# Performance work log

Measured on AMD Instinct MI355X. Metric: run time of the kernel, lower is better.

The kernel has to match this reference:

```python
import jax, jax.numpy as jnp
import numpy as np


def setup_inputs() -> dict:
    key = jax.random.key(0)
    ks = jax.random.split(key, 8)
    b, m, e, d = 8, 4096, 2048, 128
    features = jax.random.normal(ks[0], (b, m, d), dtype=jnp.float32)
    # sparse-ish binary incidence matrix (nodes x hyperedges)
    inc_mat = (jax.random.uniform(ks[1], (b, m, e)) < 0.02).astype(jnp.float32)
    s = 1.0 / np.sqrt(d)
    return {
        "features": features,
        "inc_mat": inc_mat,
        "vc_Wa": jax.random.uniform(ks[2], (d, d), minval=-s, maxval=s),
        "vc_Wp": jax.random.uniform(ks[3], (d, d), minval=-s, maxval=s),
        "vc_alpha": jnp.float32(0.5),
        "ec_Wa": jax.random.uniform(ks[4], (d, d), minval=-s, maxval=s),
        "ec_Wp": jax.random.uniform(ks[5], (d, d), minval=-s, maxval=s),
        "ec_alpha": jnp.float32(0.5),
        "n_layers": 3,
    }


def _vertex_conv(feat, inc, Wa, Wp, alpha, prev=None):
    # feat: [b,m,d], inc: [b,m,e]
    att = feat @ Wa.T                                   # [b,m,d]
    e_att = jnp.einsum('bme,bmd->bed', inc, att)        # inc^T @ att
    attw = jax.nn.softmax(e_att, axis=1)                # softmax over edges
    agg = jnp.einsum('bme,bmd->bed', inc, feat)         # collapsed bmed outer-product + contract
    ef = (agg * attw) @ Wp.T                            # [b,e,d]
    if prev is not None:
        ef = alpha * prev + (1.0 - alpha) * ef
    return ef


def _edge_conv(inc, edge_feats, Wa, Wp, alpha, prev=None):
    # NOTE: original EdgeConv computes softmax attention_weights but never uses them (dead code).
    w = jnp.einsum('bed,bme->bmd', edge_feats, inc)     # inc @ edge_feats
    nf = w @ Wp.T                                       # [b,m,d]
    if prev is not None:
        nf = alpha * prev + (1.0 - alpha) * nf
    return nf


def reference(features, inc_mat, vc_Wa, vc_Wp, vc_alpha, ec_Wa, ec_Wp, ec_alpha, n_layers):
    edge_feats = _vertex_conv(features, inc_mat, vc_Wa, vc_Wp, vc_alpha)
    node_feats = _edge_conv(inc_mat, edge_feats, ec_Wa, ec_Wp, ec_alpha)
    for _ in range(1, n_layers):
        edge_feats = _vertex_conv(features, inc_mat, vc_Wa, vc_Wp, vc_alpha, prev=edge_feats)
        node_feats = _edge_conv(inc_mat, edge_feats, ec_Wa, ec_Wp, ec_alpha, prev=node_feats)
    return node_feats, edge_feats
```

## Files before the change

kernel.cpp:

```cpp
#include <hip/hip_runtime.h>

#define BB 8
#define MM 4096
#define EE 2048
#define DD 128

typedef _Float16 f16x8 __attribute__((ext_vector_type(8)));
typedef float    f32x4 __attribute__((ext_vector_type(4)));

__global__ __launch_bounds__(256) void pack_both(const float* __restrict__ inc,
                                                 unsigned long long* __restrict__ bits,
                                                 unsigned long long* __restrict__ bitsT)
{
    const int b  = blockIdx.z;
    const int w  = threadIdx.x >> 6;
    const int lane = threadIdx.x & 63;
    const int m0 = (blockIdx.y * 4 + w) * 64;
    const int e0 = blockIdx.x * 64;
    const float* ip = inc + ((size_t)b * MM + m0) * EE + e0;

    unsigned long long wbits = 0;
    #pragma unroll
    for (int mi = 0; mi < 64; mi++){
        float v = ip[(size_t)mi * EE + lane];
        unsigned long long bal = __ballot(v != 0.0f);
        wbits = (lane == mi) ? bal : wbits;
    }
    bits[((size_t)b * MM + m0 + lane) * (EE / 64) + (e0 >> 6)] = wbits;

    unsigned long long wT = 0;
    #pragma unroll
    for (int ei = 0; ei < 64; ei++){
        unsigned long long bal = __ballot((wbits >> ei) & 1ull);
        wT = (lane == ei) ? bal : wT;
    }
    bitsT[((size_t)b * EE + e0 + lane) * (MM / 64) + (m0 >> 6)] = wT;
}

__global__ __launch_bounds__(256) void transpose_to16(const float* __restrict__ src,
                                                      _Float16* __restrict__ dst,
                                                      int R, int C)
{
    __shared__ alignas(16) float tile[64 * 67];
    const int tilesC = C >> 6;
    const int r0 = (blockIdx.x / tilesC) << 6;
    const int c0 = (blockIdx.x % tilesC) << 6;
    const float* s = src + (size_t)blockIdx.y * R * C;
    _Float16*   d = dst + (size_t)blockIdx.y * R * C;
    const int t = threadIdx.x;
    #pragma unroll
    for (int i = 0; i < 4; i++){
        int idx = t + 256 * i;
        int r = idx >> 4, c4 = idx & 15;
        float4 v = *(const float4*)(s + (size_t)(r0 + r) * C + c0 + c4 * 4);
        tile[(c4 * 4 + 0) * 67 + r] = v.x;
        tile[(c4 * 4 + 1) * 67 + r] = v.y;
        tile[(c4 * 4 + 2) * 67 + r] = v.z;
        tile[(c4 * 4 + 3) * 67 + r] = v.w;
    }
    __syncthreads();
    #pragma unroll
    for (int i = 0; i < 2; i++){
        int idx = t + 256 * i;
        int row = idx >> 3, rb = idx & 7;
        f16x8 h;
        #pragma unroll
        for (int j = 0; j < 8; j++) h[j] = (_Float16)tile[row * 67 + rb * 8 + j];
        *(f16x8*)(d + (size_t)(c0 + row) * R + r0 + rb * 8) = h;
    }
}

__global__ __launch_bounds__(256) void bitgemm1(const uint2* __restrict__ bitrows,
                                                const _Float16* __restrict__ dense,
                                                float* __restrict__ out)
{
    __shared__ alignas(16) char smem[33792];
    const int b = blockIdx.y;
    const int row0 = blockIdx.x * 64;
    const int WB = MM >> 6;
    const uint2* bp = bitrows + ((size_t)b * EE + row0) * WB;
    const _Float16* dp = dense + (size_t)b * 128 * MM;
    float* op = out + (size_t)blockIdx.z * 2097152 + ((size_t)b * EE + row0) * 128;
    const int kbase = blockIdx.z * 2048;

    const int t = threadIdx.x, lane = t & 63, w = t >> 6;
    const int fr = lane & 15, q = lane >> 4, q8 = q * 8;

    f32x4 acc[8] = {};
    uint4 rd[4];
    uint2 rb;

    auto loadg = [&](int kg){
        #pragma unroll
        for (int i = 0; i < 4; i++){
            int idx = t + 256 * i;
            int dd = idx >> 3, kb = idx & 7;
            rd[i] = *(const uint4*)(dp + (size_t)dd * MM + kg + kb * 8);
        }
        if (t < 64) rb = bp[(size_t)t * WB + (kg >> 6)];
    };
    auto stage = [&](int buf){
        _Float16* lD = (_Float16*)(smem + buf * 16384);
        uint2* lB = (uint2*)(smem + 32768 + buf * 512);
        #pragma unroll
        for (int i = 0; i < 4; i++){
            int idx = t + 256 * i;
            int dd = idx >> 3, kb = idx & 7;
            *(uint4*)&lD[dd * 64 + ((kb ^ (dd & 7)) * 8)] = rd[i];
        }
        if (t < 64) lB[t] = rb;
    };
    auto compute = [&](int buf){
        const _Float16* lD = (const _Float16*)(smem + buf * 16384);
        const uint2* lB = (const uint2*)(smem + 32768 + buf * 512);
        uint2 bw = lB[w * 16 + fr];
        #pragma unroll
        for (int h = 0; h < 2; h++){
            unsigned word = h ? bw.y : bw.x;
            unsigned byte = (word >> q8) & 0xFFu;
            f16x8 af;
            #pragma unroll
            for (int j = 0; j < 8; j++)
                af[j] = ((byte >> j) & 1u) ? (_Float16)1.0f : (_Float16)0.0f;
            #pragma unroll
            for (int c = 0; c < 8; c++){
                int drow = c * 16 + fr;
                f16x8 bf = *(const f16x8*)&lD[drow * 64 + (((h * 4 + q) ^ (drow & 7)) * 8)];
                acc[c] = __builtin_amdgcn_mfma_f32_16x16x32_f16(af, bf, acc[c], 0, 0, 0);
            }
        }
    };

    loadg(kbase); stage(0); __syncthreads();
    for (int c = 0; c < 32; c++){
        if (c + 1 < 32) loadg(kbase + (c + 1) * 64);
        compute(c & 1);
        if (c + 1 < 32) stage((c + 1) & 1);
        __syncthreads();
    }
    float* sT = (float*)smem;
    #pragma unroll
    for (int c = 0; c < 8; c++)
        #pragma unroll
        for (int reg = 0; reg < 4; reg++)
            sT[(w * 16 + q * 4 + reg) * 132 + c * 16 + fr] = acc[c][reg];
    __syncthreads();
    #pragma unroll
    for (int i = 0; i < 8; i++){
        int idx = t + 256 * i;
        int lrow = idx >> 5, c4 = idx & 31;
        float4 v = *(const float4*)&sT[lrow * 132 + c4 * 4];
        *(float4*)(op + (size_t)lrow * 128 + c4 * 4) = v;
    }
}

__global__ __launch_bounds__(256) void bitgemm2_fused(const uint2* __restrict__ bitrows,
                                                      const _Float16* __restrict__ PT,
                                                      const _Float16* __restrict__ Wc16,
                                                      float* __restrict__ node)
{
    __shared__ alignas(16) char smem[66560];
    const int b = blockIdx.y;
    const int m0 = blockIdx.x * 64;
    const int WB = EE >> 6;
    const uint2* bp = bitrows + ((size_t)b * MM + m0) * WB;
    const _Float16* dp = PT + (size_t)b * 128 * EE;
    float* op = node + ((size_t)b * MM + m0) * 128;

    const int t = threadIdx.x, lane = t & 63, w = t >> 6;
    const int fr = lane & 15, q = lane >> 4, q8 = q * 8;

    _Float16* lWc = (_Float16*)(smem + 33792);
    #pragma unroll
    for (int i = 0; i < 8; i++){
        int idx = t + 256 * i;
        int n = idx >> 4, kb = idx & 15;
        *(uint4*)&lWc[n * 128 + ((kb ^ (n & 7)) * 8)] =
            *(const uint4*)(Wc16 + (size_t)n * 128 + kb * 8);
    }

    f32x4 acc[8] = {};
    uint4 rd[4];
    uint2 rb;

    auto loadg = [&](int kg){
        #pragma unroll
        for (int i = 0; i < 4; i++){
            int idx = t + 256 * i;
            int dd = idx >> 3, kb = idx & 7;
            rd[i] = *(const uint4*)(dp + (size_t)dd * EE + kg + kb * 8);
        }
        if (t < 64) rb = bp[(size_t)t * WB + (kg >> 6)];
    };
    auto stage = [&](int buf){
        _Float16* lD = (_Float16*)(smem + buf * 16384);
        uint2* lB = (uint2*)(smem + 32768 + buf * 512);
        #pragma unroll
        for (int i = 0; i < 4; i++){
            int idx = t + 256 * i;
            int dd = idx >> 3, kb = idx & 7;
            *(uint4*)&lD[dd * 64 + ((kb ^ (dd & 7)) * 8)] = rd[i];
        }
        if (t < 64) lB[t] = rb;
    };
    auto compute = [&](int buf){
        const _Float16* lD = (const _Float16*)(smem + buf * 16384);
        const uint2* lB = (const uint2*)(smem + 32768 + buf * 512);
        uint2 bw = lB[w * 16 + fr];
        #pragma unroll
        for (int h = 0; h < 2; h++){
            unsigned word = h ? bw.y : bw.x;
            unsigned byte = (word >> q8) & 0xFFu;
            f16x8 af;
            #pragma unroll
            for (int j = 0; j < 8; j++)
                af[j] = ((byte >> j) & 1u) ? (_Float16)1.0f : (_Float16)0.0f;
            #pragma unroll
            for (int c = 0; c < 8; c++){
                int drow = c * 16 + fr;
                f16x8 bf = *(const f16x8*)&lD[drow * 64 + (((h * 4 + q) ^ (drow & 7)) * 8)];
                acc[c] = __builtin_amdgcn_mfma_f32_16x16x32_f16(af, bf, acc[c], 0, 0, 0);
            }
        }
    };

    loadg(0); stage(0); __syncthreads();
    for (int c = 0; c < 32; c++){
        if (c + 1 < 32) loadg((c + 1) * 64);
        compute(c & 1);
        if (c + 1 < 32) stage((c + 1) & 1);
        __syncthreads();
    }

    _Float16* sQ = (_Float16*)smem;
    #pragma unroll
    for (int c = 0; c < 8; c++){
        #pragma unroll
        for (int reg = 0; reg < 4; reg++){
            int row = w * 16 + q * 4 + reg;
            int col = c * 16 + fr;
            sQ[row * 128 + (((col >> 3) ^ (row & 7)) * 8) + (col & 7)] = (_Float16)acc[c][reg];
        }
    }
    f32x4 acc2[8] = {};
    #pragma unroll
    for (int kk = 0; kk < 4; kk++){
        int arow = w * 16 + fr;
        f16x8 a2 = *(const f16x8*)&sQ[arow * 128 + (((kk * 4 + q) ^ (arow & 7)) * 8)];
        #pragma unroll
        for (int c = 0; c < 8; c++){
            int n = c * 16 + fr;
            f16x8 b2 = *(const f16x8*)&lWc[n * 128 + (((kk * 4 + q) ^ (n & 7)) * 8)];
            acc2[c] = __builtin_amdgcn_mfma_f32_16x16x32_f16(a2, b2, acc2[c], 0, 0, 0);
        }
    }
    __syncthreads();
    float* sD = (float*)smem;
    #pragma unroll
    for (int c = 0; c < 8; c++)
        #pragma unroll
        for (int reg = 0; reg < 4; reg++)
            sD[(w * 16 + q * 4 + reg) * 132 + c * 16 + fr] = acc2[c][reg];
    __syncthreads();
    #pragma unroll
    for (int i = 0; i < 8; i++){
        int idx = t + 256 * i;
        int lrow = idx >> 5, c4 = idx & 31;
        float4 v = *(const float4*)&sD[lrow * 132 + c4 * 4];
        *(float4*)(op + (size_t)lrow * 128 + c4 * 4) = v;
    }
}

__global__ __launch_bounds__(256) void rowmm_sum2(const float* __restrict__ p,
                                                  const float* __restrict__ W,
                                                  float* aggOut,
                                                  float* __restrict__ C)
{
    __shared__ alignas(16) float lA[32][132];
    __shared__ alignas(16) float lW[64][140];
    const int t = threadIdx.x;
    const int row0 = blockIdx.x * 32;
    const float4* P4 = (const float4*)p;
    const float4* W4 = (const float4*)W;
    float4* A4 = (float4*)aggOut;
    const size_t SS = 2097152 / 4;

    #pragma unroll
    for (int i = 0; i < 4; i++){
        int idx = t + 256 * i;
        int r = idx >> 5, k4 = idx & 31;
        size_t gi = (size_t)(row0 + r) * 32 + k4;
        float4 a = P4[gi], b = P4[gi + SS];
        float4 s = make_float4(a.x + b.x, a.y + b.y, a.z + b.z, a.w + b.w);
        *(float4*)&lA[r][k4 * 4] = s;
        A4[gi] = s;
    }
    const int qq = t >> 5, cc = t & 31;

    #pragma unroll
    for (int ph = 0; ph < 2; ph++){
        __syncthreads();
        #pragma unroll
        for (int i = 0; i < 8; i++){
            int idx = t + 256 * i;
            int c = idx >> 5, k4 = idx & 31;
            *(float4*)&lW[c][k4 * 4] = W4[(size_t)(ph * 64 + c) * 32 + k4];
        }
        __syncthreads();
        float s[4][2] = {};
        for (int k4 = 0; k4 < 32; k4++){
            float4 w0 = *(const float4*)&lW[cc][k4 * 4];
            float4 w1 = *(const float4*)&lW[cc + 32][k4 * 4];
            #pragma unroll
            for (int j = 0; j < 4; j++){
                float4 a = *(const float4*)&lA[qq + 8 * j][k4 * 4];
                s[j][0] += a.x * w0.x + a.y * w0.y + a.z * w0.z + a.w * w0.w;
                s[j][1] += a.x * w1.x + a.y * w1.y + a.z * w1.z + a.w * w1.w;
            }
        }
        #pragma unroll
        for (int j = 0; j < 4; j++){
            size_t ro = (size_t)(row0 + qq + 8 * j) * DD + ph * 64;
            C[ro + cc]      = s[j][0];
            C[ro + cc + 32] = s[j][1];
        }
    }
}

__global__ __launch_bounds__(256) void rowmm(const float* A,
                                             const float* __restrict__ W,
                                             float* C)
{
    __shared__ alignas(16) float lA[32][132];
    __shared__ alignas(16) float lW[64][140];
    const int t = threadIdx.x;
    const int row0 = blockIdx.x * 32;
    const float4* A4 = (const float4*)A;
    const float4* W4 = (const float4*)W;

    #pragma unroll
    for (int i = 0; i < 4; i++){
        int idx = t + 256 * i;
        int r = idx >> 5, k4 = idx & 31;
        *(float4*)&lA[r][k4 * 4] = A4[(size_t)(row0 + r) * 32 + k4];
    }
    const int qq = t >> 5, cc = t & 31;

    #pragma unroll
    for (int ph = 0; ph < 2; ph++){
        __syncthreads();
        #pragma unroll
        for (int i = 0; i < 8; i++){
            int idx = t + 256 * i;
            int c = idx >> 5, k4 = idx & 31;
            *(float4*)&lW[c][k4 * 4] = W4[(size_t)(ph * 64 + c) * 32 + k4];
        }
        __syncthreads();
        float s[4][2] = {};
        for (int k4 = 0; k4 < 32; k4++){
            float4 w0 = *(const float4*)&lW[cc][k4 * 4];
            float4 w1 = *(const float4*)&lW[cc + 32][k4 * 4];
            #pragma unroll
            for (int j = 0; j < 4; j++){
                float4 a = *(const float4*)&lA[qq + 8 * j][k4 * 4];
                s[j][0] += a.x * w0.x + a.y * w0.y + a.z * w0.z + a.w * w0.w;
                s[j][1] += a.x * w1.x + a.y * w1.y + a.z * w1.z + a.w * w1.w;
            }
        }
        #pragma unroll
        for (int j = 0; j < 4; j++){
            size_t ro = (size_t)(row0 + qq + 8 * j) * DD + ph * 64;
            C[ro + cc]      = s[j][0];
            C[ro + cc + 32] = s[j][1];
        }
    }
}

__global__ __launch_bounds__(256) void wc_mm16(const float* __restrict__ eWp,
                                               const float* __restrict__ vWp,
                                               _Float16* __restrict__ Wc16)
{
    int i = blockIdx.x * 2 + (threadIdx.x >> 7);
    int j = threadIdx.x & 127;
    float acc = 0.f;
    for (int k = 0; k < 128; k++)
        acc += eWp[i * 128 + k] * vWp[k * 128 + j];
    Wc16[i * 128 + j] = (_Float16)acc;
}

__global__ __launch_bounds__(256) void sm_part(const float* __restrict__ eatt,
                                               float* __restrict__ part)
{
    const int b = blockIdx.x, slab = blockIdx.y;
    const int t = threadIdx.x;
    const int dl = t & 127, eh = t >> 7;
    const size_t base = (size_t)b * EE * DD + dl;
    const int e0 = slab * 256;
    float m = -1e30f;
    for (int s = 0; s < 128; s++)
        m = fmaxf(m, eatt[base + (size_t)(e0 + eh + 2 * s) * DD]);
    float l = 0.f;
    for (int s = 0; s < 128; s++)
        l += __expf(eatt[base + (size_t)(e0 + eh + 2 * s) * DD] - m);
    __shared__ float red[2][128][2];
    red[eh][dl][0] = m; red[eh][dl][1] = l;
    __syncthreads();
    if (t < 128){
        float m0 = red[0][t][0], l0 = red[0][t][1];
        float m1 = red[1][t][0], l1 = red[1][t][1];
        float M = fmaxf(m0, m1);
        float L = l0 * __expf(m0 - M) + l1 * __expf(m1 - M);
        float* pp = part + ((size_t)(b * 8 + slab) * DD + t) * 2;
        pp[0] = M; pp[1] = L;
    }
}

__global__ __launch_bounds__(256) void sm_apply(float* __restrict__ eatt,
                                                const float* __restrict__ agg,
                                                const float* __restrict__ part)
{
    const int b = blockIdx.x, sl = blockIdx.y;
    const int t = threadIdx.x;
    __shared__ float mv[128], iv[128];
    if (t < 128){
        float mbuf[8], lbuf[8];
        float M = -1e30f;
        #pragma unroll
        for (int s = 0; s < 8; s++){
            const float* pp = part + ((size_t)(b * 8 + s) * DD + t) * 2;
            mbuf[s] = pp[0]; lbuf[s] = pp[1];
            M = fmaxf(M, mbuf[s]);
        }
        float L = 0.f;
        #pragma unroll
        for (int s = 0; s < 8; s++) L += lbuf[s] * __expf(mbuf[s] - M);
        mv[t] = M; iv[t] = 1.f / L;
    }
    __syncthreads();
    const int dl = t & 127, eh = t >> 7;
    const size_t base = (size_t)b * EE * DD + dl;
    const int e0 = sl * 128;
    for (int s = 0; s < 64; s++){
        size_t ix = base + (size_t)(e0 + eh + 2 * s) * DD;
        eatt[ix] = agg[ix] * __expf(eatt[ix] - mv[dl]) * iv[dl];
    }
}

extern "C" void kernel_launch(void* const* d_in, const int* in_sizes, int n_in,
                              void* d_out, int out_size, void* d_ws, size_t ws_size,
                              hipStream_t stream)
{
    const float* feat = (const float*)d_in[0];
    const float* inc  = (const float*)d_in[1];
    const float* vWa  = (const float*)d_in[2];
    const float* vWp  = (const float*)d_in[3];
    const float* eWp  = (const float*)d_in[6];

    float* node_out = (float*)d_out;
    float* edge_out = node_out + (size_t)BB * MM * DD;

    char* w = (char*)d_ws;
    unsigned long long* bits  = (unsigned long long*)w;
    unsigned long long* bitsT = (unsigned long long*)(w + ((size_t)8 << 20));
    _Float16* PT = (_Float16*)(w + ((size_t)8 << 20));
    float* pk  = (float*)(w + ((size_t)16 << 20));
    float* agg = pk;
    _Float16* Wc16 = (_Float16*)(w + ((size_t)32 << 20));

    _Float16* featT = (_Float16*)node_out;
    float* eattP = node_out + 2097152;
    float* part  = edge_out;

    dim3 blk(256);

    pack_both<<<dim3(EE / 64, MM / 256, BB), blk, 0, stream>>>(inc, bits, bitsT);
    transpose_to16<<<dim3((MM / 64) * (DD / 64), BB), blk, 0, stream>>>(feat, featT, MM, DD);
    wc_mm16<<<dim3(64), blk, 0, stream>>>(eWp, vWp, Wc16);
    bitgemm1<<<dim3(EE / 64, BB, 2), blk, 0, stream>>>((const uint2*)bitsT, featT, pk);
    rowmm_sum2<<<dim3(BB * EE / 32), blk, 0, stream>>>(pk, vWa, agg, eattP);
    sm_part <<<dim3(BB, 8),  blk, 0, stream>>>(eattP, part);
    sm_apply<<<dim3(BB, 16), blk, 0, stream>>>(eattP, agg, part);
    rowmm<<<dim3(BB * EE / 32), blk, 0, stream>>>(eattP, vWp, edge_out);
    transpose_to16<<<dim3((EE / 64) * (DD / 64), BB), blk, 0, stream>>>(eattP, PT, EE, DD);
    bitgemm2_fused<<<dim3(MM / 64, BB), blk, 0, stream>>>((const uint2*)bits, PT, Wc16, node_out);
}
```

Baseline: 618.7 us.

## Fuse incidence bit-packing into first bit-GEMM with 4-way K split

Removes the separate pack_both kernel and has the first GEMM read the float incidence matrix directly. It ballots the values into bit masks, transposes them in registers for its own MFMA A operand, and writes a column-major bit layout for the second GEMM. Each block now covers 256 edges with a 4-way K split, and the partial-sum reducer is widened from 2 to 4 slices. This avoids a second pass over the bit data, but it raises register pressure (64 staged floats plus 32 accumulators, launch bound of 1 block) and gives fewer blocks per batch.

```diff
diff --git a/kernel.cpp b/kernel.cpp
--- a/kernel.cpp
+++ b/kernel.cpp
@@ -7,35 +7,6 @@
 
 typedef _Float16 f16x8 __attribute__((ext_vector_type(8)));
 typedef float    f32x4 __attribute__((ext_vector_type(4)));
-
-__global__ __launch_bounds__(256) void pack_both(const float* __restrict__ inc,
-                                                 unsigned long long* __restrict__ bits,
-                                                 unsigned long long* __restrict__ bitsT)
-{
-    const int b  = blockIdx.z;
-    const int w  = threadIdx.x >> 6;
-    const int lane = threadIdx.x & 63;
-    const int m0 = (blockIdx.y * 4 + w) * 64;
-    const int e0 = blockIdx.x * 64;
-    const float* ip = inc + ((size_t)b * MM + m0) * EE + e0;
-
-    unsigned long long wbits = 0;
-    #pragma unroll
-    for (int mi = 0; mi < 64; mi++){
-        float v = ip[(size_t)mi * EE + lane];
-        unsigned long long bal = __ballot(v != 0.0f);
-        wbits = (lane == mi) ? bal : wbits;
-    }
-    bits[((size_t)b * MM + m0 + lane) * (EE / 64) + (e0 >> 6)] = wbits;
-
-    unsigned long long wT = 0;
-    #pragma unroll
-    for (int ei = 0; ei < 64; ei++){
-        unsigned long long bal = __ballot((wbits >> ei) & 1ull);
-        wT = (lane == ei) ? bal : wT;
-    }
-    bitsT[((size_t)b * EE + e0 + lane) * (MM / 64) + (m0 >> 6)] = wT;
-}
 
 __global__ __launch_bounds__(256) void transpose_to16(const float* __restrict__ src,
                                                       _Float16* __restrict__ dst,
@@ -70,38 +41,166 @@
     }
 }
 
-__global__ __launch_bounds__(256) void bitgemm1(const uint2* __restrict__ bitrows,
-                                                const _Float16* __restrict__ dense,
-                                                float* __restrict__ out)
-{
-    __shared__ alignas(16) char smem[33792];
+__global__ __launch_bounds__(256, 1) void fused_gemm1(const float* __restrict__ inc,
+                                                      const _Float16* __restrict__ featT,
+                                                      unsigned long long* __restrict__ bitsX,
+                                                      float* __restrict__ p)
+{
+    __shared__ alignas(16) char smem[36864];
+
+    const int x = blockIdx.x;
     const int b = blockIdx.y;
-    const int row0 = blockIdx.x * 64;
-    const int WB = MM >> 6;
-    const uint2* bp = bitrows + ((size_t)b * EE + row0) * WB;
-    const _Float16* dp = dense + (size_t)b * 128 * MM;
-    float* op = out + (size_t)blockIdx.z * 2097152 + ((size_t)b * EE + row0) * 128;
-    const int kbase = blockIdx.z * 2048;
-
+    const int z = blockIdx.z;
     const int t = threadIdx.x, lane = t & 63, w = t >> 6;
     const int fr = lane & 15, q = lane >> 4, q8 = q * 8;
 
+    const int e0 = x * 256;
+    const int ew0 = e0 + w * 64;
+    const _Float16* dp = featT + (size_t)b * 128 * MM;
+    const float* ip = inc + (size_t)b * MM * EE + ew0 + lane;
+    unsigned long long* bxp = bitsX + ((size_t)b * 32 + (x * 4 + w)) * MM;
+
+    f32x4 acc[4][8] = {};
+    uint4 rd[4];
+    float val[64];
+
+    auto loadg = [&](int k0){
+        #pragma unroll
+        for (int i = 0; i < 4; i++){
+            int idx = t + 256 * i;
+            int dd = idx >> 3, kb = idx & 7;
+            rd[i] = *(const uint4*)(dp + (size_t)dd * MM + k0 + kb * 8);
+        }
+        const float* rp = ip + (size_t)k0 * EE;
+        #pragma unroll
+        for (int j = 0; j < 64; j++) val[j] = rp[(size_t)j * EE];
+    };
+    auto stage = [&](int buf, int k0){
+        _Float16* lD = (_Float16*)(smem + buf * 16384);
+        unsigned long long* lBits = (unsigned long long*)(smem + 32768 + buf * 2048);
+        #pragma unroll
+        for (int i = 0; i < 4; i++){
+            int idx = t + 256 * i;
+            int dd = idx >> 3, kb = idx & 7;
+            *(uint4*)&lD[dd * 64 + ((kb ^ (dd & 7)) * 8)] = rd[i];
+        }
+        unsigned long long wbits = 0;
+        #pragma unroll
+        for (int j = 0; j < 64; j++){
+            unsigned long long bal = __ballot(val[j] != 0.0f);
+            wbits = (lane == j) ? bal : wbits;
+        }
+        bxp[k0 + lane] = wbits;
+        unsigned long long wT = 0;
+        #pragma unroll
+        for (int ei = 0; ei < 64; ei++){
+            unsigned long long bal = __ballot((wbits >> ei) & 1ull);
+            wT = (lane == ei) ? bal : wT;
+        }
+        lBits[w * 64 + lane] = wT;
+    };
+    auto compute = [&](int buf){
+        const _Float16* lD = (const _Float16*)(smem + buf * 16384);
+        const uint2* lBits = (const uint2*)(smem + 32768 + buf * 2048);
+        uint2 bw[4];
+        f16x8 af[4][2];
+        #pragma unroll
+        for (int s = 0; s < 4; s++) bw[s] = lBits[w * 64 + s * 16 + fr];
+        #pragma unroll
+        for (int s = 0; s < 4; s++)
+            #pragma unroll
+            for (int h = 0; h < 2; h++){
+                unsigned word = h ? bw[s].y : bw[s].x;
+                unsigned byte = (word >> q8) & 0xFFu;
+                #pragma unroll
+                for (int j = 0; j < 8; j++)
+                    af[s][h][j] = ((byte >> j) & 1u) ? (_Float16)1.0f : (_Float16)0.0f;
+            }
+        #pragma unroll
+        for (int h = 0; h < 2; h++)
+            #pragma unroll
+            for (int c = 0; c < 8; c++){
+                int drow = c * 16 + fr;
+                f16x8 bf = *(const f16x8*)&lD[drow * 64 + (((h * 4 + q) ^ (drow & 7)) * 8)];
+                #pragma unroll
+                for (int s = 0; s < 4; s++)
+                    acc[s][c] = __builtin_amdgcn_mfma_f32_16x16x32_f16(af[s][h], bf, acc[s][c], 0, 0, 0);
+            }
+    };
+
+    const int kbase = z * 1024;
+    loadg(kbase); stage(0, kbase); __syncthreads();
+    for (int c = 0; c < 16; c++){
+        if (c + 1 < 16) loadg(kbase + (c + 1) * 64);
+        compute(c & 1);
+        if (c + 1 < 16) stage((c + 1) & 1, kbase + (c + 1) * 64);
+        __syncthreads();
+    }
+
+    float* sT = (float*)smem;
+    float* op = p + (size_t)z * 2097152 + ((size_t)b * EE + e0) * 128;
+    for (int ph = 0; ph < 4; ph++){
+        __syncthreads();
+        if (w == ph){
+            #pragma unroll
+            for (int s = 0; s < 4; s++)
+                #pragma unroll
+                for (int c = 0; c < 8; c++)
+                    #pragma unroll
+                    for (int reg = 0; reg < 4; reg++)
+                        sT[(s * 16 + q * 4 + reg) * 132 + c * 16 + fr] = acc[s][c][reg];
+        }
+        __syncthreads();
+        #pragma unroll
+        for (int i = 0; i < 8; i++){
+            int idx = t + 256 * i;
+            int lrow = idx >> 5, c4 = idx & 31;
+            float4 v = *(const float4*)&sT[lrow * 132 + c4 * 4];
+            *(float4*)(op + (size_t)(ph * 64 + lrow) * 128 + c4 * 4) = v;
+        }
+    }
+}
+
+__global__ __launch_bounds__(256) void bitgemm2_fused(const unsigned long long* __restrict__ bitsX,
+                                                      const _Float16* __restrict__ PT,
+                                                      const _Float16* __restrict__ Wc16,
+                                                      float* __restrict__ node)
+{
+    __shared__ alignas(16) char smem[66560];
+    const int b = blockIdx.y;
+    const int m0 = blockIdx.x * 64;
+    const unsigned long long* bxp = bitsX + (size_t)b * 32 * MM;
+    const _Float16* dp = PT + (size_t)b * 128 * EE;
+    float* op = node + ((size_t)b * MM + m0) * 128;
+
+    const int t = threadIdx.x, lane = t & 63, w = t >> 6;
+    const int fr = lane & 15, q = lane >> 4, q8 = q * 8;
+
+    _Float16* lWc = (_Float16*)(smem + 33792);
+    #pragma unroll
+    for (int i = 0; i < 8; i++){
+        int idx = t + 256 * i;
+        int n = idx >> 4, kb = idx & 15;
+        *(uint4*)&lWc[n * 128 + ((kb ^ (n & 7)) * 8)] =
+            *(const uint4*)(Wc16 + (size_t)n * 128 + kb * 8);
+    }
+
     f32x4 acc[8] = {};
     uint4 rd[4];
-    uint2 rb;
+    unsigned long long rb;
 
     auto loadg = [&](int kg){
         #pragma unroll
         for (int i = 0; i < 4; i++){
             int idx = t + 256 * i;
             int dd = idx >> 3, kb = idx & 7;
-            rd[i] = *(const uint4*)(dp + (size_t)dd * MM + kg + kb * 8);
-        }
-        if (t < 64) rb = bp[(size_t)t * WB + (kg >> 6)];
+            rd[i] = *(const uint4*)(dp + (size_t)dd * EE + kg + kb * 8);
+        }
+        if (t < 64) rb = bxp[(size_t)(kg >> 6) * MM + m0 + t];
     };
     auto stage = [&](int buf){
         _Float16* lD = (_Float16*)(smem + buf * 16384);
-        uint2* lB = (uint2*)(smem + 32768 + buf * 512);
+        unsigned long long* lB = (unsigned long long*)(smem + 32768 + buf * 512);
         #pragma unroll
         for (int i = 0; i < 4; i++){
             int idx = t + 256 * i;
@@ -131,99 +230,6 @@
         }
     };
 
-    loadg(kbase); stage(0); __syncthreads();
-    for (int c = 0; c < 32; c++){
-        if (c + 1 < 32) loadg(kbase + (c + 1) * 64);
-        compute(c & 1);
-        if (c + 1 < 32) stage((c + 1) & 1);
-        __syncthreads();
-    }
-    float* sT = (float*)smem;
-    #pragma unroll
-    for (int c = 0; c < 8; c++)
-        #pragma unroll
-        for (int reg = 0; reg < 4; reg++)
-            sT[(w * 16 + q * 4 + reg) * 132 + c * 16 + fr] = acc[c][reg];
-    __syncthreads();
-    #pragma unroll
-    for (int i = 0; i < 8; i++){
-        int idx = t + 256 * i;
-        int lrow = idx >> 5, c4 = idx & 31;
-        float4 v = *(const float4*)&sT[lrow * 132 + c4 * 4];
-        *(float4*)(op + (size_t)lrow * 128 + c4 * 4) = v;
-    }
-}
-
-__global__ __launch_bounds__(256) void bitgemm2_fused(const uint2* __restrict__ bitrows,
-                                                      const _Float16* __restrict__ PT,
-                                                      const _Float16* __restrict__ Wc16,
-                                                      float* __restrict__ node)
-{
-    __shared__ alignas(16) char smem[66560];
-    const int b = blockIdx.y;
-    const int m0 = blockIdx.x * 64;
-    const int WB = EE >> 6;
-    const uint2* bp = bitrows + ((size_t)b * MM + m0) * WB;
-    const _Float16* dp = PT + (size_t)b * 128 * EE;
-    float* op = node + ((size_t)b * MM + m0) * 128;
-
-    const int t = threadIdx.x, lane = t & 63, w = t >> 6;
-    const int fr = lane & 15, q = lane >> 4, q8 = q * 8;
-
-    _Float16* lWc = (_Float16*)(smem + 33792);
-    #pragma unroll
-    for (int i = 0; i < 8; i++){
-        int idx = t + 256 * i;
-        int n = idx >> 4, kb = idx & 15;
-        *(uint4*)&lWc[n * 128 + ((kb ^ (n & 7)) * 8)] =
-            *(const uint4*)(Wc16 + (size_t)n * 128 + kb * 8);
-    }
-
-    f32x4 acc[8] = {};
-    uint4 rd[4];
-    uint2 rb;
-
-    auto loadg = [&](int kg){
-        #pragma unroll
-        for (int i = 0; i < 4; i++){
-            int idx = t + 256 * i;
-            int dd = idx >> 3, kb = idx & 7;
-            rd[i] = *(const uint4*)(dp + (size_t)dd * EE + kg + kb * 8);
-        }
-        if (t < 64) rb = bp[(size_t)t * WB + (kg >> 6)];
-    };
-    auto stage = [&](int buf){
-        _Float16* lD = (_Float16*)(smem + buf * 16384);
-        uint2* lB = (uint2*)(smem + 32768 + buf * 512);
-        #pragma unroll
-        for (int i = 0; i < 4; i++){
-            int idx = t + 256 * i;
-            int dd = idx >> 3, kb = idx & 7;
-            *(uint4*)&lD[dd * 64 + ((kb ^ (dd & 7)) * 8)] = rd[i];
-        }
-        if (t < 64) lB[t] = rb;
-    };
-    auto compute = [&](int buf){
-        const _Float16* lD = (const _Float16*)(smem + buf * 16384);
-        const uint2* lB = (const uint2*)(smem + 32768 + buf * 512);
-        uint2 bw = lB[w * 16 + fr];
-        #pragma unroll
-        for (int h = 0; h < 2; h++){
-            unsigned word = h ? bw.y : bw.x;
-            unsigned byte = (word >> q8) & 0xFFu;
-            f16x8 af;
-            #pragma unroll
-            for (int j = 0; j < 8; j++)
-                af[j] = ((byte >> j) & 1u) ? (_Float16)1.0f : (_Float16)0.0f;
-            #pragma unroll
-            for (int c = 0; c < 8; c++){
-                int drow = c * 16 + fr;
-                f16x8 bf = *(const f16x8*)&lD[drow * 64 + (((h * 4 + q) ^ (drow & 7)) * 8)];
-                acc[c] = __builtin_amdgcn_mfma_f32_16x16x32_f16(af, bf, acc[c], 0, 0, 0);
-            }
-        }
-    };
-
     loadg(0); stage(0); __syncthreads();
     for (int c = 0; c < 32; c++){
         if (c + 1 < 32) loadg((c + 1) * 64);
@@ -271,7 +277,7 @@
     }
 }
 
-__global__ __launch_bounds__(256) void rowmm_sum2(const float* __restrict__ p,
+__global__ __launch_bounds__(256) void rowmm_sum4(const float* __restrict__ p,
                                                   const float* __restrict__ W,
                                                   float* aggOut,
                                                   float* __restrict__ C)
@@ -290,8 +296,9 @@
         int idx = t + 256 * i;
         int r = idx >> 5, k4 = idx & 31;
         size_t gi = (size_t)(row0 + r) * 32 + k4;
-        float4 a = P4[gi], b = P4[gi + SS];
-        float4 s = make_float4(a.x + b.x, a.y + b.y, a.z + b.z, a.w + b.w);
+        float4 a = P4[gi], b = P4[gi + SS], c = P4[gi + 2 * SS], d = P4[gi + 3 * SS];
+        float4 s = make_float4(a.x + b.x + c.x + d.x, a.y + b.y + c.y + d.y,
+                               a.z + b.z + c.z + d.z, a.w + b.w + c.w + d.w);
         *(float4*)&lA[r][k4 * 4] = s;
         A4[gi] = s;
     }
@@ -460,12 +467,11 @@
     float* edge_out = node_out + (size_t)BB * MM * DD;
 
     char* w = (char*)d_ws;
-    unsigned long long* bits  = (unsigned long long*)w;
-    unsigned long long* bitsT = (unsigned long long*)(w + ((size_t)8 << 20));
-    _Float16* PT = (_Float16*)(w + ((size_t)8 << 20));
-    float* pk  = (float*)(w + ((size_t)16 << 20));
+    unsigned long long* bitsX = (unsigned long long*)w;
+    float* pk  = (float*)(w + ((size_t)8 << 20));
     float* agg = pk;
-    _Float16* Wc16 = (_Float16*)(w + ((size_t)32 << 20));
+    _Float16* PT = (_Float16*)(w + ((size_t)16 << 20));
+    _Float16* Wc16 = (_Float16*)(w + ((size_t)40 << 20));
 
     _Float16* featT = (_Float16*)node_out;
     float* eattP = node_out + 2097152;
@@ -473,14 +479,13 @@
 
     dim3 blk(256);
 
-    pack_both<<<dim3(EE / 64, MM / 256, BB), blk, 0, stream>>>(inc, bits, bitsT);
     transpose_to16<<<dim3((MM / 64) * (DD / 64), BB), blk, 0, stream>>>(feat, featT, MM, DD);
     wc_mm16<<<dim3(64), blk, 0, stream>>>(eWp, vWp, Wc16);
-    bitgemm1<<<dim3(EE / 64, BB, 2), blk, 0, stream>>>((const uint2*)bitsT, featT, pk);
-    rowmm_sum2<<<dim3(BB * EE / 32), blk, 0, stream>>>(pk, vWa, agg, eattP);
+    fused_gemm1<<<dim3(EE / 256, BB, 4), blk, 0, stream>>>(inc, featT, bitsX, pk);
+    rowmm_sum4<<<dim3(BB * EE / 32), blk, 0, stream>>>(pk, vWa, agg, eattP);
     sm_part <<<dim3(BB, 8),  blk, 0, stream>>>(eattP, part);
     sm_apply<<<dim3(BB, 16), blk, 0, stream>>>(eattP, agg, part);
     rowmm<<<dim3(BB * EE / 32), blk, 0, stream>>>(eattP, vWp, edge_out);
     transpose_to16<<<dim3((EE / 64) * (DD / 64), BB), blk, 0, stream>>>(eattP, PT, EE, DD);
-    bitgemm2_fused<<<dim3(MM / 64, BB), blk, 0, stream>>>((const uint2*)bits, PT, Wc16, node_out);
-}
+    bitgemm2_fused<<<dim3(MM / 64, BB), blk, 0, stream>>>(bitsX, PT, Wc16, node_out);
+}
```

New measurement: 564.9 us. 8.7% less time.
